# Optimization experiments

Hardware: AMD Instinct MI355X
Metric: run time of the kernel (lower is better)

## Reference

```python
import jax, jax.numpy as jnp
import numpy as np

N = 262144      # total tokens
LM1 = 6         # max digit chars after the first character
D = 128         # embedding_dim
NUM_LAB = 1000
V1 = 2 * 26 + NUM_LAB  # first-level table rows (1052)


def setup_inputs() -> dict:
    key = jax.random.key(0)
    k1, k2, k3, k4, k5, k6, k7 = jax.random.split(key, 7)
    return {
        "first_chars": jax.random.randint(k1, (N,), 0, 26, dtype=jnp.int32),
        "digits": jax.random.randint(k2, (N, LM1), 0, 10, dtype=jnp.int32),
        "ndigits": jax.random.randint(k3, (N,), 0, 7, dtype=jnp.int32),
        "mods": jax.random.randint(k4, (N,), 0, 3, dtype=jnp.int32),  # 0=icd10,1=atc,2=lab
        "vals": jax.random.normal(k5, (N,), dtype=jnp.float32),
        "E1": jax.random.normal(k6, (V1, D), dtype=jnp.float32),
        "Eint": jax.random.normal(k7, (10, D), dtype=jnp.float32),
        "kappa": 2,
    }


def reference(first_chars, digits, ndigits, mods, vals, E1, Eint, kappa):
    # first-level index per modality: icd -> c+5, atc -> 2c+5, lab -> 52+code
    first_idx = jnp.where(
        mods == 0, first_chars + 5,
        jnp.where(mods == 1, first_chars * 2 + 5, 52 + first_chars))
    base = E1[first_idx]                                  # [N, D]

    # position-decayed digit accumulation: sum_i 1/(i+2)^kappa * Eint[digit_i]
    pos = jnp.arange(LM1, dtype=jnp.float32)
    w = 1.0 / (pos + 2.0) ** kappa                        # [LM1]
    mask = (jnp.arange(LM1)[None, :] < ndigits[:, None]).astype(base.dtype)
    onehot = jax.nn.one_hot(digits, 10, dtype=base.dtype)  # [N, LM1, 10]
    digit_emb = jnp.einsum("nl,nlk,kd->nd", w[None, :] * mask, onehot, Eint)

    # modality scatter: lab tokens use base * val, icd/atc use base + decayed digits
    final = jnp.where((mods == 2)[:, None], base * vals[:, None], base + digit_emb)
    return final
```

## Files before the change

### kernel.cpp

```cpp
#include <hip/hip_runtime.h>
#include <hip/hip_bf16.h>


#define LM1 6
#define D   128
#define TPT 4

__global__ __launch_bounds__(256) void hier_emb_kernel(
    const int*   __restrict__ first_chars,
    const int*   __restrict__ digits,
    const int*   __restrict__ ndigits,
    const int*   __restrict__ mods,
    const float* __restrict__ vals,
    const float* __restrict__ E1,
    const float* __restrict__ Eint,
    const int*   __restrict__ kappa_p,
    float*       __restrict__ out,
    int n)
{
    const int k = *kappa_p;

    float w[LM1];
#pragma unroll
    for (int i = 0; i < LM1; ++i) {
        float p = 1.0f;
        const float b = (float)(i + 2);
        for (int j = 0; j < k; ++j) p *= b;
        w[i] = 1.0f / p;
    }

    const long u = (long)blockIdx.x * blockDim.x + threadIdx.x;
    const int q  = (int)(u & 31);
    const int tb = (int)(u >> 5) * TPT;
    if (tb >= n) return;

    int t[TPT];
#pragma unroll
    for (int j = 0; j < TPT; ++j) {
        int tt = tb + j;
        t[j] = tt < n ? tt : (n - 1);
    }

    int mod[TPT], fc[TPT], nd[TPT];
    float vv[TPT];
#pragma unroll
    for (int j = 0; j < TPT; ++j) mod[j] = mods[t[j]];
#pragma unroll
    for (int j = 0; j < TPT; ++j) fc[j] = first_chars[t[j]];
#pragma unroll
    for (int j = 0; j < TPT; ++j) nd[j] = ndigits[t[j]];
#pragma unroll
    for (int j = 0; j < TPT; ++j) vv[j] = vals[t[j]];

    int dg[TPT][LM1];
#pragma unroll
    for (int j = 0; j < TPT; ++j) {
#pragma unroll
        for (int i = 0; i < LM1; ++i) dg[j][i] = digits[t[j] * LM1 + i];
    }

    float4 base[TPT];
#pragma unroll
    for (int j = 0; j < TPT; ++j) {
        const int fidx = (mod[j] == 0) ? (fc[j] + 5)
                       : (mod[j] == 1) ? (fc[j] * 2 + 5)
                                       : (52 + fc[j]);
        base[j] = *reinterpret_cast<const float4*>(E1 + (size_t)fidx * D + q * 4);
    }

    float4 acc[TPT];
#pragma unroll
    for (int j = 0; j < TPT; ++j) {
        if (mod[j] == 2) {
            const float v = vv[j];
            acc[j].x = base[j].x * v; acc[j].y = base[j].y * v;
            acc[j].z = base[j].z * v; acc[j].w = base[j].w * v;
        } else {
            acc[j] = base[j];
#pragma unroll
            for (int i = 0; i < LM1; ++i) {
                if (i < nd[j]) {
                    const float4 e = *reinterpret_cast<const float4*>(
                        Eint + dg[j][i] * D + q * 4);
                    acc[j].x += w[i] * e.x; acc[j].y += w[i] * e.y;
                    acc[j].z += w[i] * e.z; acc[j].w += w[i] * e.w;
                }
            }
        }
    }

#pragma unroll
    for (int j = 0; j < TPT; ++j) {
        if (tb + j < n) {
            *reinterpret_cast<float4*>(out + (size_t)(tb + j) * D + q * 4) = acc[j];
        }
    }
}

extern "C" void kernel_launch(void* const* d_in, const int* in_sizes, int n_in,
                              void* d_out, int out_size, void* d_ws, size_t ws_size,
                              hipStream_t stream) {
    const int*   first_chars = (const int*)  d_in[0];
    const int*   digits      = (const int*)  d_in[1];
    const int*   ndigits     = (const int*)  d_in[2];
    const int*   mods        = (const int*)  d_in[3];
    const float* vals        = (const float*)d_in[4];
    const float* E1          = (const float*)d_in[5];
    const float* Eint        = (const float*)d_in[6];
    const int*   kappa       = (const int*)  d_in[7];
    float*       out         = (float*)d_out;

    const int n = in_sizes[0];
    const long threads = ((long)(n + TPT - 1) / TPT) * 32;
    const int block = 256;
    const int grid = (int)((threads + block - 1) / block);

    hier_emb_kernel<<<grid, block, 0, stream>>>(
        first_chars, digits, ndigits, mods, vals, E1, Eint, kappa, out, n);
}
```

Before: 186.9 us.

## Stage Eint and per-token metadata in shared memory per block

Each block now cooperatively loads the 10x128 Eint table and its 32 tokens' metadata and digits into LDS, then synchronizes before computing. This replaces redundant per-lane global loads of metadata and Eint rows with coalesced block loads and LDS reads. The cost is one __syncthreads per block plus the 5KB Eint copy repeated in every block.

```diff
diff --git a/kernel.cpp b/kernel.cpp
--- a/kernel.cpp
+++ b/kernel.cpp
@@ -4,6 +4,7 @@
 
 #define LM1 6
 #define D   128
+#define TPB 32
 #define TPT 4
 
 __global__ __launch_bounds__(256) void hier_emb_kernel(
@@ -18,8 +19,41 @@
     float*       __restrict__ out,
     int n)
 {
+    __shared__ float sEint[10][D];
+    __shared__ int   sFidx[TPB];
+    __shared__ int   sNd[TPB];
+    __shared__ int   sMod[TPB];
+    __shared__ float sVal[TPB];
+    __shared__ int   sDig[TPB * LM1];
+
+    const int tid  = threadIdx.x;
+    const int tok0 = blockIdx.x * TPB;
+
+    {
+        const float4* src = reinterpret_cast<const float4*>(Eint);
+        float4*       dst = reinterpret_cast<float4*>(&sEint[0][0]);
+        dst[tid] = src[tid];
+        const int i2 = 256 + tid;
+        if (i2 < (10 * D) / 4) dst[i2] = src[i2];
+    }
+
+    if (tid < TPB) {
+        int tt = tok0 + tid; if (tt >= n) tt = n - 1;
+        const int mod = mods[tt];
+        const int fc  = first_chars[tt];
+        sMod[tid]  = mod;
+        sFidx[tid] = (mod == 0) ? (fc + 5) : (mod == 1) ? (fc * 2 + 5) : (52 + fc);
+        sNd[tid]   = ndigits[tt];
+        sVal[tid]  = vals[tt];
+    } else if (tid >= 64) {
+        const int i = tid - 64;
+        long gi = (long)tok0 * LM1 + i;
+        const long lim = (long)n * LM1;
+        if (gi >= lim) gi = lim - 1;
+        sDig[i] = digits[gi];
+    }
+
     const int k = *kappa_p;
-
     float w[LM1];
 #pragma unroll
     for (int i = 0; i < LM1; ++i) {
@@ -29,59 +63,36 @@
         w[i] = 1.0f / p;
     }
 
-    const long u = (long)blockIdx.x * blockDim.x + threadIdx.x;
-    const int q  = (int)(u & 31);
-    const int tb = (int)(u >> 5) * TPT;
-    if (tb >= n) return;
+    __syncthreads();
 
-    int t[TPT];
-#pragma unroll
-    for (int j = 0; j < TPT; ++j) {
-        int tt = tb + j;
-        t[j] = tt < n ? tt : (n - 1);
-    }
-
-    int mod[TPT], fc[TPT], nd[TPT];
-    float vv[TPT];
-#pragma unroll
-    for (int j = 0; j < TPT; ++j) mod[j] = mods[t[j]];
-#pragma unroll
-    for (int j = 0; j < TPT; ++j) fc[j] = first_chars[t[j]];
-#pragma unroll
-    for (int j = 0; j < TPT; ++j) nd[j] = ndigits[t[j]];
-#pragma unroll
-    for (int j = 0; j < TPT; ++j) vv[j] = vals[t[j]];
-
-    int dg[TPT][LM1];
-#pragma unroll
-    for (int j = 0; j < TPT; ++j) {
-#pragma unroll
-        for (int i = 0; i < LM1; ++i) dg[j][i] = digits[t[j] * LM1 + i];
-    }
+    const int q   = tid & 31;
+    const int ltb = (tid >> 5) * TPT;
 
     float4 base[TPT];
 #pragma unroll
     for (int j = 0; j < TPT; ++j) {
-        const int fidx = (mod[j] == 0) ? (fc[j] + 5)
-                       : (mod[j] == 1) ? (fc[j] * 2 + 5)
-                                       : (52 + fc[j]);
+        const int fidx = sFidx[ltb + j];
         base[j] = *reinterpret_cast<const float4*>(E1 + (size_t)fidx * D + q * 4);
     }
 
     float4 acc[TPT];
 #pragma unroll
     for (int j = 0; j < TPT; ++j) {
-        if (mod[j] == 2) {
-            const float v = vv[j];
+        const int lt  = ltb + j;
+        const int mod = sMod[lt];
+        if (mod == 2) {
+            const float v = sVal[lt];
             acc[j].x = base[j].x * v; acc[j].y = base[j].y * v;
             acc[j].z = base[j].z * v; acc[j].w = base[j].w * v;
         } else {
             acc[j] = base[j];
+            const int nd = sNd[lt];
 #pragma unroll
             for (int i = 0; i < LM1; ++i) {
-                if (i < nd[j]) {
-                    const float4 e = *reinterpret_cast<const float4*>(
-                        Eint + dg[j][i] * D + q * 4);
+                if (i < nd) {
+                    const int dg = sDig[lt * LM1 + i];
+                    const float4 e =
+                        *reinterpret_cast<const float4*>(&sEint[dg][q * 4]);
                     acc[j].x += w[i] * e.x; acc[j].y += w[i] * e.y;
                     acc[j].z += w[i] * e.z; acc[j].w += w[i] * e.w;
                 }
@@ -91,8 +102,9 @@
 
 #pragma unroll
     for (int j = 0; j < TPT; ++j) {
-        if (tb + j < n) {
-            *reinterpret_cast<float4*>(out + (size_t)(tb + j) * D + q * 4) = acc[j];
+        const int tok = tok0 + ltb + j;
+        if (tok < n) {
+            *reinterpret_cast<float4*>(out + (size_t)tok * D + q * 4) = acc[j];
         }
     }
 }
@@ -110,11 +122,9 @@
     const int*   kappa       = (const int*)  d_in[7];
     float*       out         = (float*)d_out;
 
-    const int n = in_sizes[0];
-    const long threads = ((long)(n + TPT - 1) / TPT) * 32;
-    const int block = 256;
-    const int grid = (int)((threads + block - 1) / block);
+    const int n    = in_sizes[0];
+    const int grid = (n + TPB - 1) / TPB;
 
-    hier_emb_kernel<<<grid, block, 0, stream>>>(
+    hier_emb_kernel<<<grid, 256, 0, stream>>>(
         first_chars, digits, ndigits, mods, vals, E1, Eint, kappa, out, n);
 }
```

After: 166.5 us. 1.12x faster.
